# Kernel optimization log

Hardware: AMD Instinct MI355X
Metric: run time of the kernel (lower is better)

The kernel has to match this reference:

```python
import jax, jax.numpy as jnp
import numpy as np

D_MODEL = 128
SEQ_LEN = 2048
WINDOW = 64
BATCH = 32


def setup_inputs() -> dict:
    key = jax.random.key(0)
    ks = jax.random.split(key, 6)
    scale = 1.0 / np.sqrt(D_MODEL)
    return {
        "x": jax.random.normal(ks[0], (BATCH, D_MODEL, SEQ_LEN), dtype=jnp.float32),
        "Wq": jax.random.normal(ks[1], (D_MODEL, D_MODEL), dtype=jnp.float32) * scale,
        "bq": jnp.zeros((D_MODEL,), dtype=jnp.float32),
        "Wk": jax.random.normal(ks[2], (D_MODEL, D_MODEL), dtype=jnp.float32) * scale,
        "bk": jnp.zeros((D_MODEL,), dtype=jnp.float32),
        "Wv": jax.random.normal(ks[3], (D_MODEL, D_MODEL), dtype=jnp.float32) * scale,
        "bv": jnp.zeros((D_MODEL,), dtype=jnp.float32),
        "Wo": jax.random.normal(ks[4], (D_MODEL, D_MODEL), dtype=jnp.float32) * scale,
        "bo": jnp.zeros((D_MODEL,), dtype=jnp.float32),
        "pos_bias": jax.random.normal(ks[5], (SEQ_LEN, SEQ_LEN), dtype=jnp.float32) * 0.02,
    }


def reference(x, Wq, bq, Wk, bk, Wv, bv, Wo, bo, pos_bias):
    # x: [N, C, L] -> [N, L, C]  (in_proj Rearrange)
    xt = jnp.swapaxes(x, 1, 2)
    L = xt.shape[1]

    q = xt @ Wq + bq  # [N, L, d]
    k = xt @ Wk + bk
    v = xt @ Wv + bv

    # AFT-Local positional bias: w_{t,t'} = pos_bias if |t-t'| < s else 0
    idx = jnp.arange(L)
    local_mask = (jnp.abs(idx[:, None] - idx[None, :]) < WINDOW).astype(xt.dtype)
    pb = pos_bias[:L, :L] * local_mask  # [L, L]

    # numerically stable exponentials (AFT paper / labml formulation)
    exp_k = jnp.exp(k - jnp.max(k, axis=1, keepdims=True))          # [N, L, d]
    exp_pb = jnp.exp(pb - jnp.max(pb, axis=1, keepdims=True))       # [L, L]

    num = jnp.einsum('ij,njd->nid', exp_pb, exp_k * v)  # [N, L, d]
    den = jnp.einsum('ij,njd->nid', exp_pb, exp_k)      # [N, L, d]

    y = jax.nn.sigmoid(q) * num / den
    out = y @ Wo + bo  # output projection

    # out_proj Rearrange: [N, L, C] -> [N, C, L]
    return jnp.swapaxes(out, 1, 2)
```

## Files before the change

### kernel.cpp

```cpp
#include <hip/hip_runtime.h>
#include <math.h>

#define NB 32
#define DM 128
#define SL 2048
#define WIN 64
#define NT  (SL / 16)
#define PADF 4
#define PADB 6
#define NTP (NT + PADF + PADB)
#define YST 132

typedef __attribute__((ext_vector_type(8))) short bf16x8;
typedef __attribute__((ext_vector_type(4))) float f32x4;

__device__ inline ushort bf16_rne(float f) {
    union { float f; unsigned u; } v; v.f = f;
    unsigned u = v.u;
    return (ushort)((u + 0x7FFFu + ((u >> 16) & 1u)) >> 16);
}
__device__ inline float bf16_to_f(ushort h) {
    union { unsigned u; float f; } v; v.u = ((unsigned)h) << 16;
    return v.f;
}


__global__ __launch_bounds__(512) void setup_kernel(
    const float* __restrict__ Wq, const float* __restrict__ Wk,
    const float* __restrict__ Wv, const float* __restrict__ Wo,
    const float* __restrict__ pos_bias,
    ushort* __restrict__ Wh, ushort* __restrict__ Wl,
    ushort* __restrict__ WB,
    ushort* __restrict__ ekTF, ushort* __restrict__ ekvTF,
    float* __restrict__ Sk, float* __restrict__ Skv)
{
    const int b = blockIdx.x;
    const int tid = threadIdx.x;
    if (b < 128) {
        const int id = b;
        const int mat = id >> 5;
        const int ct = (id & 31) >> 2, ks = id & 3;
        const int lane = tid >> 3, j = tid & 7;
        const int k = ks * 32 + (lane >> 4) * 8 + j;
        const int col = ct * 16 + (lane & 15);
        const float* W = (mat == 0) ? Wq : ((mat == 1) ? Wk : ((mat == 2) ? Wv : Wo));
        float w = W[k * DM + col];
        ushort h = bf16_rne(w);
        Wh[(size_t)id * 512 + tid] = h;
        Wl[(size_t)id * 512 + tid] = bf16_rne(w - bf16_to_f(h));
    } else if (b < 256) {
        const int it = b - 128;
        const int i0 = it * 16;
        for (int t = tid; t < 5 * 64 * 8; t += 512) {
            const int ks = t >> 9;
            const int lane = (t >> 3) & 63;
            const int jj = t & 7;
            const int m = lane & 15;
            const int k = ks * 32 + ((lane >> 4) << 3) + jj;
            const int i = i0 + m;
            const int j = i0 - 64 + k;
            const int rel = k - 64 - m;
            float val = 0.f;
            if (rel > -WIN && rel < WIN && j >= 0 && j < SL)
                val = __expf(pos_bias[(size_t)i * SL + j]) - 1.f;
            WB[(size_t)it * 2560 + t] = bf16_rne(val);
        }
    } else if (b < 576) {
        const int zb = b - 256;
        const int n = zb / 10, slot = zb % 10;
        const int jt_p = (slot < PADF) ? slot : (NT + slot);
        const size_t base = ((size_t)n * NTP + jt_p) * 2048 + (size_t)tid * 4;
        ushort4 z; z.x = 0; z.y = 0; z.z = 0; z.w = 0;
        *(ushort4*)&ekTF [base] = z;
        *(ushort4*)&ekvTF[base] = z;
    } else {
        for (int i = tid; i < NB * DM; i += 512) {
            Sk [i] = 0.f;
            Skv[i] = 0.f;
        }
    }
}

__global__ __launch_bounds__(512, 4) void qkv_kernel(
    const float* __restrict__ x,
    const ushort* __restrict__ Wh, const ushort* __restrict__ Wl,
    const float* __restrict__ bq, const float* __restrict__ bk,
    const float* __restrict__ bv,
    ushort* __restrict__ sqh, ushort* __restrict__ ekTF, ushort* __restrict__ ekvTF,
    float* __restrict__ Sk, float* __restrict__ Skv)
{
    __shared__ ushort Ah[64 * 128];
    __shared__ ushort Al[64 * 128];
    const int n = blockIdx.y, bx = blockIdx.x, l0 = bx * 64;
    const int tid = threadIdx.x;
    const int wave = tid >> 6;
    const int lane = tid & 63;

    const bf16x8* WhV = (const bf16x8*)Wh;
    const bf16x8* WlV = (const bf16x8*)Wl;

    bf16x8 bh0[3], bl0[3];
    #pragma unroll
    for (int m = 0; m < 3; ++m) {
        const int fi = ((m * 8 + wave) * 4 + 0) * 64 + lane;
        bh0[m] = WhV[fi];
        bl0[m] = WlV[fi];
    }

    {
        const int lo = lane;
        const int cq = wave;
        const int l  = l0 + lo;
        for (int cc = 0; cc < 4; ++cc) {
            const int c0 = cc * 32 + cq * 4;
            float xv[4]; ushort hh[4], ll[4];
            #pragma unroll
            for (int u = 0; u < 4; ++u)
                xv[u] = x[((size_t)n * DM + c0 + u) * SL + l];
            #pragma unroll
            for (int u = 0; u < 4; ++u) {
                hh[u] = bf16_rne(xv[u]);
                ll[u] = bf16_rne(xv[u] - bf16_to_f(hh[u]));
            }
            const int idx = ((lo >> 4) * 4 + (c0 >> 5)) * 512
                          + (((c0 >> 3) & 3) * 16 + (lo & 15)) * 8 + (c0 & 7);
            ushort4 hv; hv.x = hh[0]; hv.y = hh[1]; hv.z = hh[2]; hv.w = hh[3];
            ushort4 lv; lv.x = ll[0]; lv.y = ll[1]; lv.z = ll[2]; lv.w = ll[3];
            *(ushort4*)&Ah[idx] = hv;
            *(ushort4*)&Al[idx] = lv;
        }
    }
    __syncthreads();

    const int dcol = lane & 15;
    const int d = wave * 16 + dcol;

    f32x4 acc[3][4];
    {
        const float b0 = bq[d], b1 = bk[d], b2 = bv[d];
        #pragma unroll
        for (int lt = 0; lt < 4; ++lt) {
            acc[0][lt] = (f32x4){b0, b0, b0, b0};
            acc[1][lt] = (f32x4){b1, b1, b1, b1};
            acc[2][lt] = (f32x4){b2, b2, b2, b2};
        }
    }

    #pragma unroll
    for (int ks = 0; ks < 4; ++ks) {
        bf16x8 bh[3], bl[3];
        if (ks == 0) {
            #pragma unroll
            for (int m = 0; m < 3; ++m) { bh[m] = bh0[m]; bl[m] = bl0[m]; }
        } else {
            #pragma unroll
            for (int m = 0; m < 3; ++m) {
                const int fi = ((m * 8 + wave) * 4 + ks) * 64 + lane;
                bh[m] = WhV[fi];
                bl[m] = WlV[fi];
            }
        }
        #pragma unroll
        for (int lt = 0; lt < 4; ++lt) {
            const bf16x8 ah = *(const bf16x8*)&Ah[((lt * 4 + ks) * 64 + lane) * 8];
            const bf16x8 al = *(const bf16x8*)&Al[((lt * 4 + ks) * 64 + lane) * 8];
            #pragma unroll
            for (int m = 0; m < 3; ++m) {
                acc[m][lt] = __builtin_amdgcn_mfma_f32_16x16x32_bf16(
                    ah, bh[m], acc[m][lt], 0, 0, 0);
                acc[m][lt] = __builtin_amdgcn_mfma_f32_16x16x32_bf16(
                    al, bh[m], acc[m][lt], 0, 0, 0);
                acc[m][lt] = __builtin_amdgcn_mfma_f32_16x16x32_bf16(
                    ah, bl[m], acc[m][lt], 0, 0, 0);
            }
        }
    }

    const int lrow0 = (lane >> 4) * 4;
    float psk = 0.f, pskv = 0.f;
    #pragma unroll
    for (int lt = 0; lt < 4; ++lt) {
        const f32x4 q4 = acc[0][lt];
        const f32x4 k4 = acc[1][lt];
        const f32x4 v4 = acc[2][lt];
        ushort eh[4], zh[4];
        #pragma unroll
        for (int r = 0; r < 4; ++r) {
            const int l = l0 + lt * 16 + lrow0 + r;
            const float e = __expf(k4[r]);
            const float z = e * v4[r];
            const float s = 1.f / (1.f + __expf(-q4[r]));
            sqh[((size_t)n * SL + l) * DM + d] = (ushort)(s * 65535.f + 0.5f);
            eh[r] = bf16_rne(e);
            zh[r] = bf16_rne(z);
            psk  += e;
            pskv += z;
        }
        const size_t tb = ((size_t)n * NTP + PADF + ((l0 + lt * 16) >> 4)) * 2048
                        + (size_t)d * 16 + lrow0;
        ushort4 ev; ev.x = eh[0]; ev.y = eh[1]; ev.z = eh[2]; ev.w = eh[3];
        ushort4 zv; zv.x = zh[0]; zv.y = zh[1]; zv.z = zh[2]; zv.w = zh[3];
        *(ushort4*)&ekTF [tb] = ev;
        *(ushort4*)&ekvTF[tb] = zv;
    }
    {
        float a = psk, b = pskv;
        a += __shfl_xor(a, 16, 64); a += __shfl_xor(a, 32, 64);
        b += __shfl_xor(b, 16, 64); b += __shfl_xor(b, 32, 64);
        if (lane < 16) {
            const int o = n * DM + d;
            atomicAdd(&Sk [o], a);
            atomicAdd(&Skv[o], b);
        }
    }
}

__global__ __launch_bounds__(256, 4) void band_out_kernel(
    const ushort* __restrict__ ekTF, const ushort* __restrict__ ekvTF,
    const ushort* __restrict__ WB,
    const float* __restrict__ Sk, const float* __restrict__ Skv,
    const ushort* __restrict__ sqg,
    const ushort* __restrict__ Wh, const ushort* __restrict__ Wl,
    const float* __restrict__ bo, float* __restrict__ out)
{
    __shared__ __align__(16) union {
        float ylds[64 * YST];
        float ot[128 * 65];
    } u;

    const int bid = blockIdx.x;
    const int xcd = bid & 7;
    const int slot = bid >> 3;
    const int nsub = slot >> 5;
    const int itg  = slot & 31;
    const int n = xcd * 4 + nsub;
    const int wave = threadIdx.x >> 6;
    const int lane = threadIdx.x & 63;
    const int it = itg * 4 + wave;
    const int i0 = it * 16;
    const int l0 = itg * 64;

    const int dcol = lane & 15;
    const int jgrp8 = (lane >> 4) << 3;

    f32x4 den[8], num[8];
    #pragma unroll
    for (int dt = 0; dt < 8; ++dt) {
        const float sk = Sk [n * DM + dt * 16 + dcol];
        const float sv = Skv[n * DM + dt * 16 + dcol];
        den[dt] = (f32x4){sk, sk, sk, sk};
        num[dt] = (f32x4){sv, sv, sv, sv};
    }

    const bf16x8* WBv = (const bf16x8*)(WB + (size_t)it * 2560);
    const size_t lsel = (size_t)(lane >> 5) * 2048 + (size_t)((lane >> 4) & 1) * 8
                      + (size_t)dcol * 16;
    #pragma unroll
    for (int ks = 0; ks < 5; ++ks) {
        const bf16x8 a = WBv[ks * 64 + lane];
        const size_t tb = ((size_t)n * NTP + it + 2 * ks) * 2048 + lsel;
        #pragma unroll
        for (int dt = 0; dt < 8; ++dt) {
            const size_t rbase = tb + (size_t)dt * 256;
            const bf16x8 bden = *(const bf16x8*)(ekTF  + rbase);
            const bf16x8 bnum = *(const bf16x8*)(ekvTF + rbase);
            den[dt] = __builtin_amdgcn_mfma_f32_16x16x32_bf16(a, bden, den[dt], 0, 0, 0);
            num[dt] = __builtin_amdgcn_mfma_f32_16x16x32_bf16(a, bnum, num[dt], 0, 0, 0);
        }
    }

    const int irow0 = (lane >> 4) << 2;
    #pragma unroll
    for (int dt = 0; dt < 8; ++dt) {
        const int d = dt * 16 + dcol;
        #pragma unroll
        for (int r = 0; r < 4; ++r) {
            const int i = i0 + irow0 + r;
            const float s = (float)sqg[((size_t)n * SL + i) * DM + d] * (1.f / 65535.f);
            const float y = s * num[dt][r] / den[dt][r];
            u.ylds[(wave * 16 + irow0 + r) * YST + d] = y;
        }
    }

    float af[4][8];
    {
        const int arow = wave * 16 + (lane & 15);
        #pragma unroll
        for (int ks = 0; ks < 4; ++ks) {
            const int base = arow * YST + ks * 32 + jgrp8;
            const float4 a0 = *(const float4*)&u.ylds[base];
            const float4 a1 = *(const float4*)&u.ylds[base + 4];
            af[ks][0] = a0.x; af[ks][1] = a0.y; af[ks][2] = a0.z; af[ks][3] = a0.w;
            af[ks][4] = a1.x; af[ks][5] = a1.y; af[ks][6] = a1.z; af[ks][7] = a1.w;
        }
    }
    __syncthreads();

    bf16x8 yh[4], yl[4];
    #pragma unroll
    for (int ks = 0; ks < 4; ++ks) {
        #pragma unroll
        for (int t = 0; t < 8; ++t) {
            const float v = af[ks][t];
            const ushort h = bf16_rne(v);
            yh[ks][t] = (short)h;
            yl[ks][t] = (short)bf16_rne(v - bf16_to_f(h));
        }
    }

    f32x4 acc[8];
    #pragma unroll
    for (int ct = 0; ct < 8; ++ct) {
        const float b0 = bo[ct * 16 + dcol];
        acc[ct] = (f32x4){b0, b0, b0, b0};
    }

    const bf16x8* WhV = (const bf16x8*)Wh;
    const bf16x8* WlV = (const bf16x8*)Wl;
    #pragma unroll
    for (int ks = 0; ks < 4; ++ks) {
        #pragma unroll
        for (int ct = 0; ct < 8; ++ct) {
            const int fi = ((24 + ct) * 4 + ks) * 64 + lane;
            const bf16x8 bh = WhV[fi];
            const bf16x8 bl = WlV[fi];
            acc[ct] = __builtin_amdgcn_mfma_f32_16x16x32_bf16(yh[ks], bh, acc[ct], 0, 0, 0);
            acc[ct] = __builtin_amdgcn_mfma_f32_16x16x32_bf16(yl[ks], bh, acc[ct], 0, 0, 0);
            acc[ct] = __builtin_amdgcn_mfma_f32_16x16x32_bf16(yh[ks], bl, acc[ct], 0, 0, 0);
        }
    }

    #pragma unroll
    for (int ct = 0; ct < 8; ++ct) {
        const int c = ct * 16 + dcol;
        #pragma unroll
        for (int r = 0; r < 4; ++r)
            u.ot[c * 65 + wave * 16 + irow0 + r] = acc[ct][r];
    }
    __syncthreads();

    const int tid = threadIdx.x;
    #pragma unroll
    for (int rep = 0; rep < 32; ++rep) {
        const int e = rep * 256 + tid;
        const int c = e >> 6, l = e & 63;
        out[((size_t)n * DM + c) * SL + l0 + l] = u.ot[c * 65 + l];
    }
}

extern "C" void kernel_launch(void* const* d_in, const int* in_sizes, int n_in,
                              void* d_out, int out_size, void* d_ws, size_t ws_size,
                              hipStream_t stream)
{
    const float* x        = (const float*)d_in[0];
    const float* Wq       = (const float*)d_in[1];
    const float* bq       = (const float*)d_in[2];
    const float* Wk       = (const float*)d_in[3];
    const float* bk       = (const float*)d_in[4];
    const float* Wv       = (const float*)d_in[5];
    const float* bv       = (const float*)d_in[6];
    const float* Wo       = (const float*)d_in[7];
    const float* bo       = (const float*)d_in[8];
    const float* pos_bias = (const float*)d_in[9];
    float* out = (float*)d_out;

    const size_t NLD = (size_t)NB * SL * DM;
    ushort* sqh   = (ushort*)d_ws;
    ushort* ekTF  = sqh   + NLD;
    ushort* ekvTF = ekTF  + (size_t)NB * NTP * 2048;
    ushort* WB    = ekvTF + (size_t)NB * NTP * 2048;
    float*  Sk    = (float*)(WB + (size_t)128 * 2560);
    float*  Skv   = Sk   + (size_t)NB * DM;
    ushort* Wh    = (ushort*)(Skv + (size_t)NB * DM);
    ushort* Wl    = Wh + (size_t)4 * DM * DM;

    setup_kernel   <<<dim3(577),     512, 0, stream>>>(Wq, Wk, Wv, Wo, pos_bias,
                                                       Wh, Wl, WB, ekTF, ekvTF,
                                                       Sk, Skv);
    qkv_kernel     <<<dim3(32, NB),  512, 0, stream>>>(x, Wh, Wl, bq, bk, bv,
                                                       sqh, ekTF, ekvTF, Sk, Skv);
    band_out_kernel<<<dim3(NB * 32), 256, 0, stream>>>(ekTF, ekvTF, WB, Sk, Skv, sqh,
                                                       Wh, Wl, bo, out);
}
```

Before: 160.8 us.

## Replace atomic column sums with per-block partials and move padding zeroing

Instead of zeroing Sk/Skv and accumulating them with global atomics, each qkv block writes its partial column sums to a per-block slot, and each band_out block reduces the 32 partials into shared memory before starting. Zeroing of the padded ek tiles moves from setup_kernel into the first qkv blocks, and the WB band-weight build is split across twice as many setup blocks. The WB fragments are also preloaded into registers earlier. This removes atomic contention and the zero-init work, at the cost of a redundant 32-way reduction in every band_out block plus a __syncthreads.

```diff
diff --git a/kernel.cpp b/kernel.cpp
--- a/kernel.cpp
+++ b/kernel.cpp
@@ -30,9 +30,7 @@
     const float* __restrict__ Wv, const float* __restrict__ Wo,
     const float* __restrict__ pos_bias,
     ushort* __restrict__ Wh, ushort* __restrict__ Wl,
-    ushort* __restrict__ WB,
-    ushort* __restrict__ ekTF, ushort* __restrict__ ekvTF,
-    float* __restrict__ Sk, float* __restrict__ Skv)
+    ushort* __restrict__ WB)
 {
     const int b = blockIdx.x;
     const int tid = threadIdx.x;
@@ -48,10 +46,13 @@
         ushort h = bf16_rne(w);
         Wh[(size_t)id * 512 + tid] = h;
         Wl[(size_t)id * 512 + tid] = bf16_rne(w - bf16_to_f(h));
-    } else if (b < 256) {
-        const int it = b - 128;
+    } else {
+        const int idx = b - 128;
+        const int it = idx >> 1;
+        const int half = idx & 1;
         const int i0 = it * 16;
-        for (int t = tid; t < 5 * 64 * 8; t += 512) {
+        const int tend = half * 1280 + 1280;
+        for (int t = half * 1280 + tid; t < tend; t += 512) {
             const int ks = t >> 9;
             const int lane = (t >> 3) & 63;
             const int jj = t & 7;
@@ -65,19 +66,6 @@
                 val = __expf(pos_bias[(size_t)i * SL + j]) - 1.f;
             WB[(size_t)it * 2560 + t] = bf16_rne(val);
         }
-    } else if (b < 576) {
-        const int zb = b - 256;
-        const int n = zb / 10, slot = zb % 10;
-        const int jt_p = (slot < PADF) ? slot : (NT + slot);
-        const size_t base = ((size_t)n * NTP + jt_p) * 2048 + (size_t)tid * 4;
-        ushort4 z; z.x = 0; z.y = 0; z.z = 0; z.w = 0;
-        *(ushort4*)&ekTF [base] = z;
-        *(ushort4*)&ekvTF[base] = z;
-    } else {
-        for (int i = tid; i < NB * DM; i += 512) {
-            Sk [i] = 0.f;
-            Skv[i] = 0.f;
-        }
     }
 }
 
@@ -87,7 +75,7 @@
     const float* __restrict__ bq, const float* __restrict__ bk,
     const float* __restrict__ bv,
     ushort* __restrict__ sqh, ushort* __restrict__ ekTF, ushort* __restrict__ ekvTF,
-    float* __restrict__ Sk, float* __restrict__ Skv)
+    float* __restrict__ Pk, float* __restrict__ Pkv)
 {
     __shared__ ushort Ah[64 * 128];
     __shared__ ushort Al[64 * 128];
@@ -95,6 +83,14 @@
     const int tid = threadIdx.x;
     const int wave = tid >> 6;
     const int lane = tid & 63;
+
+    if (bx < 10) {
+        const int jt_p = (bx < PADF) ? bx : (NT + bx);
+        const size_t zb = ((size_t)n * NTP + jt_p) * 2048 + (size_t)tid * 4;
+        ushort4 z; z.x = 0; z.y = 0; z.z = 0; z.w = 0;
+        *(ushort4*)&ekTF [zb] = z;
+        *(ushort4*)&ekvTF[zb] = z;
+    }
 
     const bf16x8* WhV = (const bf16x8*)Wh;
     const bf16x8* WlV = (const bf16x8*)Wl;
@@ -208,9 +204,9 @@
         a += __shfl_xor(a, 16, 64); a += __shfl_xor(a, 32, 64);
         b += __shfl_xor(b, 16, 64); b += __shfl_xor(b, 32, 64);
         if (lane < 16) {
-            const int o = n * DM + d;
-            atomicAdd(&Sk [o], a);
-            atomicAdd(&Skv[o], b);
+            const size_t o = ((size_t)n * 32 + bx) * DM + d;
+            Pk [o] = a;
+            Pkv[o] = b;
         }
     }
 }
@@ -218,7 +214,7 @@
 __global__ __launch_bounds__(256, 4) void band_out_kernel(
     const ushort* __restrict__ ekTF, const ushort* __restrict__ ekvTF,
     const ushort* __restrict__ WB,
-    const float* __restrict__ Sk, const float* __restrict__ Skv,
+    const float* __restrict__ Pk, const float* __restrict__ Pkv,
     const ushort* __restrict__ sqg,
     const ushort* __restrict__ Wh, const ushort* __restrict__ Wl,
     const float* __restrict__ bo, float* __restrict__ out)
@@ -227,6 +223,7 @@
         float ylds[64 * YST];
         float ot[128 * 65];
     } u;
+    __shared__ float SkL[DM], SkvL[DM];
 
     const int bid = blockIdx.x;
     const int xcd = bid & 7;
@@ -243,21 +240,36 @@
     const int dcol = lane & 15;
     const int jgrp8 = (lane >> 4) << 3;
 
+    const bf16x8* WBv = (const bf16x8*)(WB + (size_t)it * 2560);
+    bf16x8 aWB[5];
+    #pragma unroll
+    for (int ks = 0; ks < 5; ++ks) aWB[ks] = WBv[ks * 64 + lane];
+
+    {
+        const int tdd = threadIdx.x & 127;
+        const float* P = (threadIdx.x < 128) ? Pk : Pkv;
+        float s = 0.f;
+        #pragma unroll
+        for (int seg = 0; seg < 32; ++seg)
+            s += P[((size_t)n * 32 + seg) * DM + tdd];
+        if (threadIdx.x < 128) SkL[tdd] = s; else SkvL[tdd] = s;
+    }
+    __syncthreads();
+
     f32x4 den[8], num[8];
     #pragma unroll
     for (int dt = 0; dt < 8; ++dt) {
-        const float sk = Sk [n * DM + dt * 16 + dcol];
-        const float sv = Skv[n * DM + dt * 16 + dcol];
+        const float sk = SkL [dt * 16 + dcol];
+        const float sv = SkvL[dt * 16 + dcol];
         den[dt] = (f32x4){sk, sk, sk, sk};
         num[dt] = (f32x4){sv, sv, sv, sv};
     }
 
-    const bf16x8* WBv = (const bf16x8*)(WB + (size_t)it * 2560);
     const size_t lsel = (size_t)(lane >> 5) * 2048 + (size_t)((lane >> 4) & 1) * 8
                       + (size_t)dcol * 16;
     #pragma unroll
     for (int ks = 0; ks < 5; ++ks) {
-        const bf16x8 a = WBv[ks * 64 + lane];
+        const bf16x8 a = aWB[ks];
         const size_t tb = ((size_t)n * NTP + it + 2 * ks) * 2048 + lsel;
         #pragma unroll
         for (int dt = 0; dt < 8; ++dt) {
@@ -369,16 +381,15 @@
     ushort* ekTF  = sqh   + NLD;
     ushort* ekvTF = ekTF  + (size_t)NB * NTP * 2048;
     ushort* WB    = ekvTF + (size_t)NB * NTP * 2048;
-    float*  Sk    = (float*)(WB + (size_t)128 * 2560);
-    float*  Skv   = Sk   + (size_t)NB * DM;
-    ushort* Wh    = (ushort*)(Skv + (size_t)NB * DM);
+    float*  Pk    = (float*)(WB + (size_t)128 * 2560);
+    float*  Pkv   = Pk   + (size_t)NB * 32 * DM;
+    ushort* Wh    = (ushort*)(Pkv + (size_t)NB * 32 * DM);
     ushort* Wl    = Wh + (size_t)4 * DM * DM;
 
-    setup_kernel   <<<dim3(577),     512, 0, stream>>>(Wq, Wk, Wv, Wo, pos_bias,
-                                                       Wh, Wl, WB, ekTF, ekvTF,
-                                                       Sk, Skv);
+    setup_kernel   <<<dim3(384),     512, 0, stream>>>(Wq, Wk, Wv, Wo, pos_bias,
+                                                       Wh, Wl, WB);
     qkv_kernel     <<<dim3(32, NB),  512, 0, stream>>>(x, Wh, Wl, bq, bk, bv,
-                                                       sqh, ekTF, ekvTF, Sk, Skv);
-    band_out_kernel<<<dim3(NB * 32), 256, 0, stream>>>(ekTF, ekvTF, WB, Sk, Skv, sqh,
+                                                       sqh, ekTF, ekvTF, Pk, Pkv);
+    band_out_kernel<<<dim3(NB * 32), 256, 0, stream>>>(ekTF, ekvTF, WB, Pk, Pkv, sqh,
                                                        Wh, Wl, bo, out);
 }
```

Result: no change. 162.1 us (+0.8%).
